# Optimization experiments

Hardware: AMD Instinct MI355X
Metric: run time of the kernel (lower is better)

## Reference

```python
import jax, jax.numpy as jnp
import numpy as np

B, T, N, V, C, E = 64, 100, 25, 128, 128, 64
EPS = 1e-5


def setup_inputs() -> dict:
    key = jax.random.key(0)
    ks = jax.random.split(key, 6)
    x = jax.random.normal(ks[0], (B, T, N, V), jnp.float32)
    edge_index = jax.random.randint(ks[1], (2, E), 0, N, dtype=jnp.int64)
    W1 = jax.random.normal(ks[2], (V, C), jnp.float32) * (1.0 / np.sqrt(V))
    b1 = jnp.zeros((C,), jnp.float32)
    W2 = jax.random.normal(ks[3], (C, C), jnp.float32) * (1.0 / np.sqrt(C))
    b2 = jnp.zeros((C,), jnp.float32)
    gamma = jnp.ones((T,), jnp.float32)
    beta = jnp.zeros((T,), jnp.float32)
    return {"x": x, "edge_index": edge_index, "W1": W1, "b1": b1,
            "W2": W2, "b2": b2, "gamma": gamma, "beta": beta}


def _gcn_norm(edge_index, n):
    # GCNConv default: add self-loops, symmetric D^{-1/2} A_hat D^{-1/2} norm.
    loop = jnp.arange(n, dtype=edge_index.dtype)
    src = jnp.concatenate([edge_index[0], loop])  # [E + N]
    tgt = jnp.concatenate([edge_index[1], loop])
    deg = jnp.zeros((n,), jnp.float32).at[tgt].add(1.0)
    dis = jax.lax.rsqrt(deg)  # deg >= 1 due to self-loops
    return src, tgt, dis[src] * dis[tgt]


def _gcn_layer(h, W, b, src, tgt, norm):
    # h: [G, N, Cin] -> [G, N, Cout]; linear then gather-scale-scatter aggregate.
    h = jnp.einsum('gnc,cd->gnd', h, W)
    msg = h[:, src, :] * norm[None, :, None]          # [G, E+N, Cout]
    out = jnp.zeros_like(h).at[:, tgt, :].add(msg)    # scatter-add to targets
    return out + b


def reference(x, edge_index, W1, b1, W2, b2, gamma, beta):
    Bv, Tv, Nv, Vv = x.shape
    h = x.reshape(Bv * Tv, Nv, Vv)  # B*T independent graphs, shared edge_index
    src, tgt, norm = _gcn_norm(edge_index, Nv)
    h = _gcn_layer(h, W1, b1, src, tgt, norm)
    h = _gcn_layer(h, W2, b2, src, tgt, norm)
    y = h.reshape(Bv, Tv, Nv, -1)
    # BatchNorm2d(T) in training mode: batch stats over (B, N, C) per T-channel.
    mean = y.mean(axis=(0, 2, 3), keepdims=True)
    var = y.var(axis=(0, 2, 3), keepdims=True)  # biased, matches torch normalization
    y = (y - mean) * jax.lax.rsqrt(var + EPS)
    y = y * gamma[None, :, None, None] + beta[None, :, None, None]
    return jax.nn.relu(y)
```

## Files before the change

### kernel.cpp

```cpp
#include <hip/hip_runtime.h>

#define T_DIM   100
#define N_NODES 25
#define C_DIM   128
#define B_DIM   64
#define G_TOTAL 6400
#define GNV     3200
#define CNT_PER_T 204800.0f

#define WS_A2   0
#define WS_RS1  640
#define WS_BW   768
#define WS_SUM  1024
#define WS_SSQ  1152
#define WS_W12T 2048

typedef __attribute__((ext_vector_type(8))) short short8;
typedef __attribute__((ext_vector_type(4))) float f32x4;

__device__ __forceinline__ unsigned short f2bf(float f) {
  unsigned int u = __float_as_uint(f);
  u += 0x7FFFu + ((u >> 16) & 1u);
  return (unsigned short)(u >> 16);
}

__global__ void k_prep(const int* __restrict__ edge, float* __restrict__ wsf) {
  __shared__ float sA[N_NODES][N_NODES];
  __shared__ float sdeg[N_NODES];
  __shared__ float sdis[N_NODES];
  const int tid = threadIdx.x;

  if (tid < N_NODES) sdeg[tid] = 0.f;
  for (int j = tid; j < N_NODES * N_NODES; j += 256) ((float*)sA)[j] = 0.f;
  __syncthreads();
  if (tid < 64) atomicAdd(&sdeg[edge[64 + tid]], 1.f);
  __syncthreads();
  if (tid < N_NODES) sdis[tid] = rsqrtf(sdeg[tid] + 1.f);
  __syncthreads();
  if (tid < 64) {
    int s = edge[tid], tg = edge[64 + tid];
    atomicAdd(&sA[tg][s], sdis[s] * sdis[tg]);
  }
  __syncthreads();
  if (tid < N_NODES) atomicAdd(&sA[tid][tid], sdis[tid] * sdis[tid]);
  __syncthreads();
  for (int j = tid; j < N_NODES * N_NODES; j += 256) {
    int n = j / N_NODES, m = j - n * N_NODES;
    float acc = 0.f;
    for (int k = 0; k < N_NODES; k++) acc = fmaf(sA[n][k], sA[k][m], acc);
    wsf[WS_A2 + j] = acc;
  }
  if (tid < N_NODES) {
    float rs = 0.f;
    for (int m = 0; m < N_NODES; m++) rs += sA[tid][m];
    wsf[WS_RS1 + tid] = rs;
  }
  if (tid < T_DIM) { wsf[WS_SUM + tid] = 0.f; wsf[WS_SSQ + tid] = 0.f; }
}

__global__ void k_wprep(const float* __restrict__ W1, const float* __restrict__ W2,
                        const float* __restrict__ b1, float* __restrict__ wsf) {
  int j = blockIdx.x * 256 + threadIdx.x;
  int c = j & 127, v = j >> 7;
  float acc = 0.f;
#pragma unroll 8
  for (int u = 0; u < 128; u++) acc = fmaf(W1[v * 128 + u], W2[u * 128 + c], acc);
  ((unsigned short*)(wsf + WS_W12T))[c * 128 + v] = f2bf(acc);
  if (j < 128) {
    float a2 = 0.f;
    for (int u = 0; u < 128; u++) a2 = fmaf(W2[u * 128 + j], b1[u], a2);
    wsf[WS_BW + j] = a2;
  }
}

__global__ __launch_bounds__(256, 4) void k_main(const float* __restrict__ x,
                                                 const float* __restrict__ b2,
                                                 const float* __restrict__ wsc,
                                                 float* __restrict__ stats,
                                                 float* __restrict__ out) {
  __shared__ __align__(16) unsigned short XA[112 * 128];
  __shared__ float rs1[32];
  __shared__ float red[8];
  const int tid = threadIdx.x;
  const int bid = blockIdx.x;
  const int t = bid % T_DIM;
  const int bq = bid / T_DIM;
  const int wv = tid >> 6, lane = tid & 63, quad = lane >> 4, l16 = lane & 15;

  if (tid < N_NODES) rs1[tid] = wsc[WS_RS1 + tid];
  for (int j = tid; j < 12 * 128; j += 256)
    XA[(100 + (j >> 7)) * 128 + (j & 127)] = 0;

  {
    const int v = tid & 127;
    const int gl0 = tid >> 7;
    const float* A2 = wsc + WS_A2;
    const int g0 = (bq * 4 + gl0) * T_DIM + t;
    const float* xp0 = x + g0 * GNV + v;
    const float* xp1 = xp0 + 2 * T_DIM * GNV;
    float x0[25], x1[25];
#pragma unroll
    for (int m = 0; m < 25; m++) { x0[m] = xp0[m * 128]; x1[m] = xp1[m * 128]; }
    for (int n = 0; n < 25; n++) {
      float a0 = 0.f, a1 = 0.f;
#pragma unroll
      for (int m = 0; m < 25; m++) {
        float w = A2[n * 25 + m];
        a0 = fmaf(w, x0[m], a0);
        a1 = fmaf(w, x1[m], a1);
      }
      int r0 = gl0 * 25 + n, r1 = r0 + 50;
      XA[r0 * 128 + (v ^ ((r0 & 15) << 3))] = f2bf(a0);
      XA[r1 * 128 + (v ^ ((r1 & 15) << 3))] = f2bf(a1);
    }
  }

  short8 bfr[2][4];
  {
    const unsigned short* Wg = (const unsigned short*)(wsc + WS_W12T);
#pragma unroll
    for (int nt = 0; nt < 2; nt++) {
      const short8* rp = (const short8*)&Wg[(wv * 32 + nt * 16 + l16) * 128];
#pragma unroll
      for (int ks = 0; ks < 4; ks++) bfr[nt][ks] = rp[(ks << 2) | quad];
    }
  }
  __syncthreads();

  f32x4 acc[7][2];
#pragma unroll
  for (int mt = 0; mt < 7; mt++)
#pragma unroll
    for (int nt = 0; nt < 2; nt++)
#pragma unroll
      for (int r = 0; r < 4; r++) acc[mt][nt][r] = 0.f;

#pragma unroll
  for (int ks = 0; ks < 4; ks++) {
    const int cc = (ks << 2) | quad;
#pragma unroll
    for (int mt = 0; mt < 7; mt++) {
      int arow = mt * 16 + l16;
      short8 afr = *(const short8*)&XA[arow * 128 + ((cc ^ (arow & 15)) << 3)];
#pragma unroll
      for (int nt = 0; nt < 2; nt++)
        acc[mt][nt] = __builtin_amdgcn_mfma_f32_16x16x32_bf16(afr, bfr[nt][ks], acc[mt][nt], 0, 0, 0);
    }
  }

  const int c0i = wv * 32 + l16;
  const float bw0 = wsc[WS_BW + c0i], bw1 = wsc[WS_BW + c0i + 16];
  const float bb0 = b2[c0i], bb1 = b2[c0i + 16];
  float sum = 0.f, ssq = 0.f;
#pragma unroll
  for (int mt = 0; mt < 7; mt++) {
#pragma unroll
    for (int r = 0; r < 4; r++) {
      int row = mt * 16 + quad * 4 + r;
      if (row < 100) {
        int gl = row / 25;
        int n = row - gl * 25;
        float rsn = rs1[n];
        int g = (bq * 4 + gl) * T_DIM + t;
        int ob = g * GNV + n * 128 + c0i;
        float v0 = acc[mt][0][r] + rsn * bw0 + bb0;
        float v1 = acc[mt][1][r] + rsn * bw1 + bb1;
        out[ob] = v0;
        out[ob + 16] = v1;
        sum += v0 + v1;
        ssq += v0 * v0 + v1 * v1;
      }
    }
  }
#pragma unroll
  for (int off = 32; off > 0; off >>= 1) {
    sum += __shfl_down(sum, off, 64);
    ssq += __shfl_down(ssq, off, 64);
  }
  if (lane == 0) { red[wv] = sum; red[4 + wv] = ssq; }
  __syncthreads();
  if (tid == 0) {
    atomicAdd(&stats[t], red[0] + red[1] + red[2] + red[3]);
    atomicAdd(&stats[128 + t], red[4] + red[5] + red[6] + red[7]);
  }
}

#define NORM_T4   5120000
#define NORM_STR  1280000
__global__ __launch_bounds__(256) void k_norm(float* __restrict__ out,
                                              const float* __restrict__ stats,
                                              const float* __restrict__ gamma,
                                              const float* __restrict__ beta) {
  const int i0 = blockIdx.x * 256 + threadIdx.x;
  const float inv = 1.f / CNT_PER_T;
  float4 h[4];
  float g[4], bb[4];
  int base[4];
#pragma unroll
  for (int k = 0; k < 4; k++) {
    int i4 = i0 + k * NORM_STR;
    base[k] = i4 * 4;
    int t = (base[k] / GNV) % T_DIM;
    float s = stats[t], q = stats[128 + t];
    float mean = s * inv;
    float var = fmaf(q, inv, -mean * mean);
    float rstd = rsqrtf(var + 1e-5f);
    g[k] = gamma[t] * rstd;
    bb[k] = fmaf(-mean, g[k], beta[t]);
    h[k] = *(const float4*)(out + base[k]);
  }
#pragma unroll
  for (int k = 0; k < 4; k++) {
    float4 v = h[k];
    v.x = fmaxf(fmaf(v.x, g[k], bb[k]), 0.f);
    v.y = fmaxf(fmaf(v.y, g[k], bb[k]), 0.f);
    v.z = fmaxf(fmaf(v.z, g[k], bb[k]), 0.f);
    v.w = fmaxf(fmaf(v.w, g[k], bb[k]), 0.f);
    *(float4*)(out + base[k]) = v;
  }
}

extern "C" void kernel_launch(void* const* d_in, const int* in_sizes, int n_in,
                              void* d_out, int out_size, void* d_ws, size_t ws_size,
                              hipStream_t stream) {
  const float* x     = (const float*)d_in[0];
  const int*   edge  = (const int*)d_in[1];
  const float* W1    = (const float*)d_in[2];
  const float* b1    = (const float*)d_in[3];
  const float* W2    = (const float*)d_in[4];
  const float* b2    = (const float*)d_in[5];
  const float* gamma = (const float*)d_in[6];
  const float* beta  = (const float*)d_in[7];
  float* out = (float*)d_out;
  float* wsf = (float*)d_ws;

  k_prep<<<1, 256, 0, stream>>>(edge, wsf);
  k_wprep<<<64, 256, 0, stream>>>(W1, W2, b1, wsf);
  k_main<<<G_TOTAL / 4, 256, 0, stream>>>(x, b2, wsf, wsf + WS_SUM, out);
  k_norm<<<NORM_STR / 256, 256, 0, stream>>>(out, wsf + WS_SUM, gamma, beta);
}
```

Baseline: 215.0 us.

## Move graph aggregation after feature GEMM and run it on MFMA

The A^2 node-aggregation was done with scalar FMAs on x before the feature GEMM. It now runs after the GEMM as a second bf16 MFMA, using A^2 padded to 32x32, with the GEMM output restaged through LDS in a transposed layout. The two prep kernels are also merged into one launch. This reduces per-thread scalar FMA work and register pressure, but adds an LDS round trip, extra syncs and another bf16 rounding of intermediate values.

```diff
diff --git a/kernel.cpp b/kernel.cpp
--- a/kernel.cpp
+++ b/kernel.cpp
@@ -8,13 +8,16 @@
 #define GNV     3200
 #define CNT_PER_T 204800.0f
 
-#define WS_A2   0
+#define WS_A2P  0
 #define WS_RS1  640
 #define WS_BW   768
 #define WS_SUM  1024
 #define WS_SSQ  1152
 #define WS_W12T 2048
 
+#define YSTR  36
+#define YGSTR (128 * YSTR)
+
 typedef __attribute__((ext_vector_type(8))) short short8;
 typedef __attribute__((ext_vector_type(4))) float f32x4;
 
@@ -23,15 +26,36 @@
   u += 0x7FFFu + ((u >> 16) & 1u);
   return (unsigned short)(u >> 16);
 }
-
-__global__ void k_prep(const int* __restrict__ edge, float* __restrict__ wsf) {
-  __shared__ float sA[N_NODES][N_NODES];
+__device__ __forceinline__ unsigned int pack2bf(float a, float b) {
+  return (unsigned int)f2bf(a) | ((unsigned int)f2bf(b) << 16);
+}
+
+__global__ void k_pre(const int* __restrict__ edge, const float* __restrict__ W1,
+                      const float* __restrict__ W2, const float* __restrict__ b1,
+                      float* __restrict__ wsf) {
+  __shared__ float sA[N_NODES * N_NODES];
+  __shared__ float sA2[N_NODES * N_NODES];
   __shared__ float sdeg[N_NODES];
   __shared__ float sdis[N_NODES];
   const int tid = threadIdx.x;
 
+  if (blockIdx.x < 64) {
+    int j = blockIdx.x * 256 + tid;
+    int c = j & 127, v = j >> 7;
+    float acc = 0.f;
+#pragma unroll 8
+    for (int u = 0; u < 128; u++) acc = fmaf(W1[v * 128 + u], W2[u * 128 + c], acc);
+    ((unsigned short*)(wsf + WS_W12T))[c * 128 + v] = f2bf(acc);
+    if (j < 128) {
+      float a2 = 0.f;
+      for (int u = 0; u < 128; u++) a2 = fmaf(W2[u * 128 + j], b1[u], a2);
+      wsf[WS_BW + j] = a2;
+    }
+    return;
+  }
+
   if (tid < N_NODES) sdeg[tid] = 0.f;
-  for (int j = tid; j < N_NODES * N_NODES; j += 256) ((float*)sA)[j] = 0.f;
+  for (int j = tid; j < N_NODES * N_NODES; j += 256) sA[j] = 0.f;
   __syncthreads();
   if (tid < 64) atomicAdd(&sdeg[edge[64 + tid]], 1.f);
   __syncthreads();
@@ -39,38 +63,29 @@
   __syncthreads();
   if (tid < 64) {
     int s = edge[tid], tg = edge[64 + tid];
-    atomicAdd(&sA[tg][s], sdis[s] * sdis[tg]);
-  }
-  __syncthreads();
-  if (tid < N_NODES) atomicAdd(&sA[tid][tid], sdis[tid] * sdis[tid]);
+    atomicAdd(&sA[tg * N_NODES + s], sdis[s] * sdis[tg]);
+  }
+  __syncthreads();
+  if (tid < N_NODES) atomicAdd(&sA[tid * N_NODES + tid], sdis[tid] * sdis[tid]);
   __syncthreads();
   for (int j = tid; j < N_NODES * N_NODES; j += 256) {
     int n = j / N_NODES, m = j - n * N_NODES;
     float acc = 0.f;
-    for (int k = 0; k < N_NODES; k++) acc = fmaf(sA[n][k], sA[k][m], acc);
-    wsf[WS_A2 + j] = acc;
+    for (int k = 0; k < N_NODES; k++) acc = fmaf(sA[n * N_NODES + k], sA[k * N_NODES + m], acc);
+    sA2[j] = acc;
+  }
+  __syncthreads();
+  for (int j = tid; j < 1024; j += 256) {
+    int m = j >> 5, k = j & 31;
+    float v = (m < N_NODES && k < N_NODES) ? sA2[m * N_NODES + k] : 0.f;
+    ((unsigned short*)(wsf + WS_A2P))[j] = f2bf(v);
   }
   if (tid < N_NODES) {
     float rs = 0.f;
-    for (int m = 0; m < N_NODES; m++) rs += sA[tid][m];
+    for (int m = 0; m < N_NODES; m++) rs += sA[tid * N_NODES + m];
     wsf[WS_RS1 + tid] = rs;
   }
   if (tid < T_DIM) { wsf[WS_SUM + tid] = 0.f; wsf[WS_SSQ + tid] = 0.f; }
-}
-
-__global__ void k_wprep(const float* __restrict__ W1, const float* __restrict__ W2,
-                        const float* __restrict__ b1, float* __restrict__ wsf) {
-  int j = blockIdx.x * 256 + threadIdx.x;
-  int c = j & 127, v = j >> 7;
-  float acc = 0.f;
-#pragma unroll 8
-  for (int u = 0; u < 128; u++) acc = fmaf(W1[v * 128 + u], W2[u * 128 + c], acc);
-  ((unsigned short*)(wsf + WS_W12T))[c * 128 + v] = f2bf(acc);
-  if (j < 128) {
-    float a2 = 0.f;
-    for (int u = 0; u < 128; u++) a2 = fmaf(W2[u * 128 + j], b1[u], a2);
-    wsf[WS_BW + j] = a2;
-  }
 }
 
 __global__ __launch_bounds__(256, 4) void k_main(const float* __restrict__ x,
@@ -78,7 +93,9 @@
                                                  const float* __restrict__ wsc,
                                                  float* __restrict__ stats,
                                                  float* __restrict__ out) {
-  __shared__ __align__(16) unsigned short XA[112 * 128];
+  __shared__ __align__(16) unsigned short LB[4 * YGSTR];
+  __shared__ float sBW[128];
+  __shared__ float sB2[128];
   __shared__ float rs1[32];
   __shared__ float red[8];
   const int tid = threadIdx.x;
@@ -87,31 +104,33 @@
   const int bq = bid / T_DIM;
   const int wv = tid >> 6, lane = tid & 63, quad = lane >> 4, l16 = lane & 15;
 
-  if (tid < N_NODES) rs1[tid] = wsc[WS_RS1 + tid];
-  for (int j = tid; j < 12 * 128; j += 256)
-    XA[(100 + (j >> 7)) * 128 + (j & 127)] = 0;
+  if (tid < 128) {
+    sBW[tid] = wsc[WS_BW + tid];
+    if (tid < N_NODES) rs1[tid] = wsc[WS_RS1 + tid];
+  } else {
+    sB2[tid - 128] = b2[tid - 128];
+  }
+  for (int j = tid; j < 12 * 128; j += 256) {
+    int pr = j >> 7;
+    int g = pr >> 2, rr = pr & 3;
+    g = pr / 3; rr = pr - g * 3;
+    LB[(g * 28 + 25 + rr) * 128 + (j & 127)] = 0;
+  }
 
   {
     const int v = tid & 127;
     const int gl0 = tid >> 7;
-    const float* A2 = wsc + WS_A2;
     const int g0 = (bq * 4 + gl0) * T_DIM + t;
     const float* xp0 = x + g0 * GNV + v;
     const float* xp1 = xp0 + 2 * T_DIM * GNV;
     float x0[25], x1[25];
 #pragma unroll
     for (int m = 0; m < 25; m++) { x0[m] = xp0[m * 128]; x1[m] = xp1[m * 128]; }
+#pragma unroll
     for (int n = 0; n < 25; n++) {
-      float a0 = 0.f, a1 = 0.f;
-#pragma unroll
-      for (int m = 0; m < 25; m++) {
-        float w = A2[n * 25 + m];
-        a0 = fmaf(w, x0[m], a0);
-        a1 = fmaf(w, x1[m], a1);
-      }
-      int r0 = gl0 * 25 + n, r1 = r0 + 50;
-      XA[r0 * 128 + (v ^ ((r0 & 15) << 3))] = f2bf(a0);
-      XA[r1 * 128 + (v ^ ((r1 & 15) << 3))] = f2bf(a1);
+      int r0 = gl0 * 28 + n, r1 = (gl0 + 2) * 28 + n;
+      LB[r0 * 128 + (v ^ ((r0 & 15) << 3))] = f2bf(x0[n]);
+      LB[r1 * 128 + (v ^ ((r1 & 15) << 3))] = f2bf(x1[n]);
     }
   }
 
@@ -141,37 +160,87 @@
 #pragma unroll
     for (int mt = 0; mt < 7; mt++) {
       int arow = mt * 16 + l16;
-      short8 afr = *(const short8*)&XA[arow * 128 + ((cc ^ (arow & 15)) << 3)];
+      short8 afr = *(const short8*)&LB[arow * 128 + ((cc ^ (arow & 15)) << 3)];
 #pragma unroll
       for (int nt = 0; nt < 2; nt++)
         acc[mt][nt] = __builtin_amdgcn_mfma_f32_16x16x32_bf16(afr, bfr[nt][ks], acc[mt][nt], 0, 0, 0);
     }
   }
-
-  const int c0i = wv * 32 + l16;
-  const float bw0 = wsc[WS_BW + c0i], bw1 = wsc[WS_BW + c0i + 16];
-  const float bb0 = b2[c0i], bb1 = b2[c0i + 16];
+  __syncthreads();
+
+#pragma unroll
+  for (int mt = 0; mt < 7; mt++) {
+    int row0 = mt * 16 + quad * 4;
+    int g = row0 / 28;
+    int rl = row0 - g * 28;
+#pragma unroll
+    for (int nt = 0; nt < 2; nt++) {
+      int c = wv * 32 + nt * 16 + l16;
+      uint2 p;
+      p.x = pack2bf(acc[mt][nt][0], acc[mt][nt][1]);
+      p.y = pack2bf(acc[mt][nt][2], acc[mt][nt][3]);
+      *(uint2*)&LB[g * YGSTR + c * YSTR + rl] = p;
+    }
+  }
+  {
+    uint2 z; z.x = 0u; z.y = 0u;
+    for (int j = tid; j < 512; j += 256) {
+      int g = j >> 7, c = j & 127;
+      *(uint2*)&LB[g * YGSTR + c * YSTR + 28] = z;
+    }
+  }
+  __syncthreads();
+
+  const unsigned short* A2p = (const unsigned short*)(wsc + WS_A2P);
+  short8 a2f[2];
+#pragma unroll
+  for (int mt2 = 0; mt2 < 2; mt2++)
+    a2f[mt2] = *(const short8*)&A2p[(mt2 * 16 + l16) * 32 + quad * 8];
+
+  const int obase = ((bq * 4 + wv) * T_DIM + t) * GNV;
   float sum = 0.f, ssq = 0.f;
 #pragma unroll
-  for (int mt = 0; mt < 7; mt++) {
-#pragma unroll
-    for (int r = 0; r < 4; r++) {
-      int row = mt * 16 + quad * 4 + r;
-      if (row < 100) {
-        int gl = row / 25;
-        int n = row - gl * 25;
-        float rsn = rs1[n];
-        int g = (bq * 4 + gl) * T_DIM + t;
-        int ob = g * GNV + n * 128 + c0i;
-        float v0 = acc[mt][0][r] + rsn * bw0 + bb0;
-        float v1 = acc[mt][1][r] + rsn * bw1 + bb1;
-        out[ob] = v0;
-        out[ob + 16] = v1;
-        sum += v0 + v1;
-        ssq += v0 * v0 + v1 * v1;
+  for (int half = 0; half < 2; half++) {
+    f32x4 acc2[2][4];
+#pragma unroll
+    for (int mt2 = 0; mt2 < 2; mt2++)
+#pragma unroll
+      for (int nt = 0; nt < 4; nt++)
+#pragma unroll
+        for (int r = 0; r < 4; r++) acc2[mt2][nt][r] = 0.f;
+
+#pragma unroll
+    for (int nt = 0; nt < 4; nt++) {
+      int c = (half * 4 + nt) * 16 + l16;
+      int base = wv * YGSTR + c * YSTR + quad * 8;
+      uint2 lo = *(const uint2*)&LB[base];
+      uint2 hi = *(const uint2*)&LB[base + 4];
+      uint4 w; w.x = lo.x; w.y = lo.y; w.z = hi.x; w.w = hi.y;
+      short8 bf = __builtin_bit_cast(short8, w);
+#pragma unroll
+      for (int mt2 = 0; mt2 < 2; mt2++)
+        acc2[mt2][nt] = __builtin_amdgcn_mfma_f32_16x16x32_bf16(a2f[mt2], bf, acc2[mt2][nt], 0, 0, 0);
+    }
+#pragma unroll
+    for (int mt2 = 0; mt2 < 2; mt2++) {
+#pragma unroll
+      for (int nt = 0; nt < 4; nt++) {
+        int c = (half * 4 + nt) * 16 + l16;
+        float bw = sBW[c], bb = sB2[c];
+#pragma unroll
+        for (int r = 0; r < 4; r++) {
+          int m = mt2 * 16 + quad * 4 + r;
+          if (m < N_NODES) {
+            float v = acc2[mt2][nt][r] + rs1[m] * bw + bb;
+            out[obase + m * 128 + c] = v;
+            sum += v;
+            ssq += v * v;
+          }
+        }
       }
     }
   }
+
 #pragma unroll
   for (int off = 32; off > 0; off >>= 1) {
     sum += __shfl_down(sum, off, 64);
@@ -185,7 +254,6 @@
   }
 }
 
-#define NORM_T4   5120000
 #define NORM_STR  1280000
 __global__ __launch_bounds__(256) void k_norm(float* __restrict__ out,
                                               const float* __restrict__ stats,
@@ -234,8 +302,7 @@
   float* out = (float*)d_out;
   float* wsf = (float*)d_ws;
 
-  k_prep<<<1, 256, 0, stream>>>(edge, wsf);
-  k_wprep<<<64, 256, 0, stream>>>(W1, W2, b1, wsf);
+  k_pre<<<65, 256, 0, stream>>>(edge, W1, W2, b1, wsf);
   k_main<<<G_TOTAL / 4, 256, 0, stream>>>(x, b2, wsf, wsf + WS_SUM, out);
   k_norm<<<NORM_STR / 256, 256, 0, stream>>>(out, wsf + WS_SUM, gamma, beta);
 }
```

New measurement: 200.8 us. 1.07x faster.
